# Kernel tuning notes

Measured on AMD Instinct MI355X. Metric: run time of the kernel, lower is better.

Reference implementation:

```python
import jax, jax.numpy as jnp
import numpy as np


def _gcn(A, x, W, b):
    # GCNConv(improved=True): add_remaining_self_loops(fill=2), symmetric normalization.
    n = A.shape[0]
    idx = jnp.arange(n)
    d = jnp.diagonal(A)
    Ahat = A.at[idx, idx].set(jnp.where(d == 0, 2.0, d))  # keep existing self-loop weights
    dinv = 1.0 / jnp.sqrt(Ahat.sum(axis=1))
    return (Ahat * dinv[:, None] * dinv[None, :]) @ (x @ W) + b


def _augment(A):
    # GraphUNet.augment_adj: add self loops, A @ A (spspmm), remove self loops.
    n = A.shape[0]
    idx = jnp.arange(n)
    A1 = A.at[idx, idx].add(1.0)
    return (A1 @ A1).at[idx, idx].set(0.0)


def _pool(A, x, p, k):
    # TopKPooling with tanh nonlinearity.
    score = jnp.tanh((x @ p) / jnp.linalg.norm(p))
    vals, perm = jax.lax.top_k(score, k)
    return A[perm][:, perm], x[perm] * vals[:, None], perm


def _gat(mask, x, W, a_src, a_dst, b, heads, c, concat):
    # GATConv, eval mode (attention dropout inactive). mask[dst, src] includes self loops.
    n = x.shape[0]
    h = (x @ W).reshape(n, heads, c)
    es = jnp.einsum('shc,hc->sh', h, a_src)
    ed = jnp.einsum('dhc,hc->dh', h, a_dst)
    logits = jax.nn.leaky_relu(ed[:, None, :] + es[None, :, :], 0.2)  # [dst, src, h]
    logits = jnp.where(mask[:, :, None], logits, jnp.finfo(logits.dtype).min)
    alpha = jax.nn.softmax(logits, axis=1)  # softmax over sources per destination
    out = jnp.einsum('dsh,shc->dhc', alpha, h)
    out = out.reshape(n, heads * c) if concat else out.mean(axis=1)
    return out + b


def setup_inputs() -> dict:
    key = jax.random.key(0)
    ks = jax.random.split(key, 34)
    N, E, IN, H, OUT, HEADS = 4096, 65536, 3, 64, 128, 4
    r = lambda k, s: jax.random.normal(k, s, jnp.float32) * 0.1
    inp = {}
    inp['x'] = jax.random.normal(ks[0], (N, IN), jnp.float32)
    inp['edge_index'] = jax.random.randint(ks[1], (2, E), 0, N)
    inp['unet_w0'] = r(ks[2], (IN, H)); inp['unet_b0'] = jnp.zeros((H,), jnp.float32)
    inp['unet_w1'] = r(ks[3], (H, H)); inp['unet_b1'] = jnp.zeros((H,), jnp.float32)
    inp['unet_w2'] = r(ks[4], (H, H)); inp['unet_b2'] = jnp.zeros((H,), jnp.float32)
    inp['unet_w3'] = r(ks[5], (H, H)); inp['unet_b3'] = jnp.zeros((H,), jnp.float32)
    inp['pool_p1'] = r(ks[6], (H,)); inp['pool_p2'] = r(ks[7], (H,)); inp['pool_p3'] = r(ks[8], (H,))
    inp['up_w0'] = r(ks[9], (H, H)); inp['up_b0'] = jnp.zeros((H,), jnp.float32)
    inp['up_w1'] = r(ks[10], (H, H)); inp['up_b1'] = jnp.zeros((H,), jnp.float32)
    inp['up_w2'] = r(ks[11], (H, OUT)); inp['up_b2'] = jnp.zeros((OUT,), jnp.float32)
    inp['ln_g'] = jnp.ones((OUT,), jnp.float32); inp['ln_b'] = jnp.zeros((OUT,), jnp.float32)
    inp['res_w'] = r(ks[12], (OUT, OUT)); inp['res_b'] = jnp.zeros((OUT,), jnp.float32)
    inp['gat1_w'] = r(ks[13], (OUT, HEADS * OUT))
    inp['gat1_asrc'] = r(ks[14], (HEADS, OUT)); inp['gat1_adst'] = r(ks[15], (HEADS, OUT))
    inp['gat1_b'] = jnp.zeros((HEADS * OUT,), jnp.float32)
    inp['gat2_w'] = r(ks[16], (HEADS * OUT, OUT))
    inp['gat2_asrc'] = r(ks[17], (1, OUT)); inp['gat2_adst'] = r(ks[18], (1, OUT))
    inp['gat2_b'] = jnp.zeros((OUT,), jnp.float32)
    return inp


def reference(x, edge_index, unet_w0, unet_b0, unet_w1, unet_b1, unet_w2, unet_b2,
              unet_w3, unet_b3, pool_p1, pool_p2, pool_p3, up_w0, up_b0, up_w1, up_b1,
              up_w2, up_b2, ln_g, ln_b, res_w, res_b, gat1_w, gat1_asrc, gat1_adst,
              gat1_b, gat2_w, gat2_asrc, gat2_adst, gat2_b):
    n0 = x.shape[0]
    # Dense weighted adjacency A[dst, src]; duplicate edges accumulate weight (scatter-add).
    A0 = jnp.zeros((n0, n0), x.dtype).at[edge_index[1], edge_index[0]].add(1.0)
    # ---- GraphUNet down path ----
    x0 = jax.nn.relu(_gcn(A0, x, unet_w0, unet_b0))
    k1 = (n0 + 1) // 2
    A1, h1, perm1 = _pool(_augment(A0), x0, pool_p1, k1)
    x1 = jax.nn.relu(_gcn(A1, h1, unet_w1, unet_b1))
    k2 = (k1 + 1) // 2
    A2, h2, perm2 = _pool(_augment(A1), x1, pool_p2, k2)
    x2 = jax.nn.relu(_gcn(A2, h2, unet_w2, unet_b2))
    k3 = (k2 + 1) // 2
    A3, h3, perm3 = _pool(_augment(A2), x2, pool_p3, k3)
    x3 = jax.nn.relu(_gcn(A3, h3, unet_w3, unet_b3))
    # ---- up path (sum_res=True) ----
    h = x2 + jnp.zeros_like(x2).at[perm3].set(x3)
    h = jax.nn.relu(_gcn(A2, h, up_w0, up_b0))
    h = x1 + jnp.zeros_like(x1).at[perm2].set(h)
    h = jax.nn.relu(_gcn(A1, h, up_w1, up_b1))
    h = x0 + jnp.zeros_like(x0).at[perm1].set(h)
    h = _gcn(A0, h, up_w2, up_b2)  # last up conv: no activation -> [n0, 128]
    # ---- LayerNorm(eps=1e-6) ----
    mu = h.mean(-1, keepdims=True)
    var = ((h - mu) ** 2).mean(-1, keepdims=True)
    u = (h - mu) / jnp.sqrt(var + 1e-6) * ln_g + ln_b
    residual = u @ res_w + res_b
    mask = (A0 > 0) | jnp.eye(n0, dtype=bool)  # GATConv adds self loops
    g = jax.nn.elu(_gat(mask, u, gat1_w, gat1_asrc, gat1_adst, gat1_b, 4, 128, True))
    g = _gat(mask, g, gat2_w, gat2_asrc, gat2_adst, gat2_b, 1, 128, False)
    return g + residual
```

## Files before the change

### kernel.cpp

```cpp
#include <hip/hip_runtime.h>
#include <math.h>


#define TPB 256
#define LDK 88
#define MAXN 128

typedef __attribute__((ext_vector_type(8))) short bf16x8;
typedef __attribute__((ext_vector_type(4))) float f32x4;

__device__ inline ushort f32_to_bf16(float v) {
    unsigned b = __float_as_uint(v);
    return (ushort)((b + 0x7FFF + ((b >> 16) & 1)) >> 16);
}
__device__ inline float bf2f(ushort u) { return __uint_as_float(((unsigned)u) << 16); }

__global__ void csr_init(int n, int* __restrict__ nbr, float* __restrict__ awt) {
    int id = blockIdx.x * TPB + threadIdx.x;
    if (id >= n * MAXN) return;
    int i = id >> 7, slot = id & (MAXN - 1);
    nbr[id] = (slot == 0) ? i : -1;
    awt[id] = (slot == 0) ? 1.0f : 0.0f;
}

__global__ void csr_insert(const int* __restrict__ ei, int E, int* __restrict__ nbr,
                           float* __restrict__ awt, int* __restrict__ deg,
                           int* __restrict__ diag) {
    int e = blockIdx.x * TPB + threadIdx.x;
    if (e >= E) return;
    int src = ei[e];
    int dst = ei[E + e];
    atomicAdd(&deg[dst], 1);
    if (src == dst) diag[src] = 1;
    int base = dst * MAXN;
    for (int p = 0; p < MAXN; ++p) {
        int cur = nbr[base + p];
        if (cur == src) { atomicAdd(&awt[base + p], 1.0f); break; }
        if (cur == -1) {
            int old = atomicCAS(&nbr[base + p], -1, src);
            if (old == -1 || old == src) { atomicAdd(&awt[base + p], 1.0f); break; }
        }
    }
}

__global__ void csr_finalize(const int* __restrict__ nbr, const int* __restrict__ deg,
                             const int* __restrict__ diag, int n, int* __restrict__ acnt,
                             float* __restrict__ dinv, float* __restrict__ selfw) {
    int i = blockIdx.x * TPB + threadIdx.x;
    if (i >= n) return;
    int cnt = 0;
    for (int p = 0; p < MAXN; ++p) {
        if (nbr[i * MAXN + p] == -1) break;
        ++cnt;
    }
    acnt[i] = cnt;
    float sw = diag[i] ? 0.f : 2.f;
    dinv[i] = 1.0f / sqrtf((float)deg[i] + sw);
    selfw[i] = sw;
}

__global__ void xw_gemm(const float* __restrict__ xin, const float* __restrict__ W,
                        float* __restrict__ C, int n, int fin, int f) {
    __shared__ float sW[64 * 128];
    int tid = threadIdx.x;
    for (int t = tid; t < fin * f; t += TPB) sW[t] = W[t];
    __syncthreads();
    int rpb = TPB / f;
    int r = blockIdx.x * rpb + tid / f;
    int c = tid - (tid / f) * f;
    if (r >= n) return;
    const float* xr = xin + (size_t)r * fin;
    float acc = 0.f;
    for (int k = 0; k < fin; ++k) acc += xr[k] * sW[k * f + c];
    C[(size_t)r * f + c] = acc;
}

__global__ void spmv_gcn(const int* __restrict__ nbr, const float* __restrict__ awt,
                         const int* __restrict__ acnt, const float* __restrict__ xw,
                         const float* __restrict__ dinv, const float* __restrict__ selfw,
                         const float* __restrict__ bias, float* __restrict__ out,
                         int f, int relu) {
    int i = blockIdx.x;
    int o = threadIdx.x;
    __shared__ int sj[MAXN];
    __shared__ float sw_[MAXN];
    int cnt = acnt[i];
    for (int a = o; a < cnt; a += blockDim.x) {
        sj[a] = nbr[i * MAXN + a];
        sw_[a] = awt[i * MAXN + a];
    }
    __syncthreads();
    if (o >= f) return;
    float sum = 0.f;
    for (int a = 0; a < cnt; ++a) {
        int j = sj[a];
        sum += sw_[a] * (xw[(size_t)j * f + o] * dinv[j]);
    }
    float yi = xw[(size_t)i * f + o] * dinv[i];
    sum -= yi;
    float v = dinv[i] * (sum + selfw[i] * yi) + bias[o];
    if (relu) v = fmaxf(v, 0.f);
    out[(size_t)i * f + o] = v;
}

__global__ void score_kernel2(const float* __restrict__ x, const float* __restrict__ p,
                              float* __restrict__ s, int n) {
    int i = blockIdx.x * TPB + threadIdx.x;
    if (i >= n) return;
    float a = 0.f, nrm = 0.f;
    for (int c = 0; c < 64; ++c) {
        float pc = p[c];
        nrm += pc * pc;
        a += x[(size_t)i * 64 + c] * pc;
    }
    s[i] = tanhf(a / sqrtf(nrm));
}

__global__ void rank_count(const float* __restrict__ s, int n, int* __restrict__ rank) {
    __shared__ float sj[256];
    int i = blockIdx.x * 256 + threadIdx.x;
    int j0 = blockIdx.y * 256;
    sj[threadIdx.x] = s[j0 + threadIdx.x];
    float si = s[i];
    __syncthreads();
    int r = 0;
#pragma unroll 8
    for (int jj = 0; jj < 256; ++jj) {
        float v = sj[jj];
        r += (v > si) || (v == si && (j0 + jj) < i);
    }
    atomicAdd(&rank[i], r);
}

__global__ void scatter_topk_all(const float* __restrict__ s, const int* __restrict__ rank,
                                 int n, int k, int* __restrict__ perm,
                                 float* __restrict__ vals, int* __restrict__ invp) {
    int i = blockIdx.x * TPB + threadIdx.x;
    if (i >= n) return;
    int r = rank[i];
    if (r < k) { perm[r] = i; vals[r] = s[i]; invp[i] = r; }
    else invp[i] = -1;
}

__global__ void gather_feat(const float* __restrict__ x, const int* __restrict__ perm,
                            const float* __restrict__ vals, int k, int f, float* __restrict__ h) {
    int id = blockIdx.x * TPB + threadIdx.x;
    if (id >= k * f) return;
    int r = id / f, c = id - r * f;
    h[id] = x[(size_t)perm[r] * f + c] * vals[r];
}

__global__ void spgemm_aug(const int* __restrict__ nbr, const float* __restrict__ awt,
                           const int* __restrict__ acnt, const int* __restrict__ perm,
                           const int* __restrict__ invp, int k,
                           ushort* __restrict__ Chi, ushort* __restrict__ Clo,
                           float* __restrict__ dinv, float* __restrict__ selfw) {
    __shared__ float row[2048];
    int r = blockIdx.x, tid = threadIdx.x;
    int pi = perm[r];
    for (int j = tid; j < k; j += TPB) row[j] = 0.f;
    __syncthreads();
    int cnt = acnt[pi];
    for (int a = 0; a < cnt; ++a) {
        int t = nbr[pi * MAXN + a];
        float w1 = awt[pi * MAXN + a];
        int c2 = acnt[t];
        for (int b = tid; b < c2; b += TPB) {
            int s = nbr[t * MAXN + b];
            int j = invp[s];
            if (j >= 0) atomicAdd(&row[j], w1 * awt[t * MAXN + b]);
        }
    }
    __syncthreads();
    float psum = 0.f;
    for (int j = tid; j < k; j += TPB) {
        float v = (j == r) ? 0.f : row[j];
        psum += v;
        ushort hi = f32_to_bf16(v);
        size_t o = (size_t)r * k + j;
        Chi[o] = hi;
        Clo[o] = f32_to_bf16(v - bf2f(hi));
    }
    for (int o = 32; o; o >>= 1) psum += __shfl_xor(psum, o);
    __shared__ float sh[4];
    if ((tid & 63) == 0) sh[tid >> 6] = psum;
    __syncthreads();
    if (tid == 0) {
        float tot = sh[0] + sh[1] + sh[2] + sh[3];
        dinv[r] = 1.0f / sqrtf(tot + 2.0f);
        selfw[r] = 2.0f;
    }
}

__global__ void transpose_aug_hl(const ushort* __restrict__ Ahi, const ushort* __restrict__ Alo,
                                 ushort* __restrict__ T, int n) {
    __shared__ float tile[64][65];
    int c0 = blockIdx.x * 64, r0 = blockIdx.y * 64;
    for (int t = threadIdx.x; t < 4096; t += TPB) {
        int r = t >> 6, c = t & 63;
        size_t o = (size_t)(r0 + r) * n + (c0 + c);
        float v = bf2f(Ahi[o]) + bf2f(Alo[o]);
        if (r0 + r == c0 + c) v += 1.0f;
        tile[c][r] = v;
    }
    __syncthreads();
    for (int t = threadIdx.x; t < 4096; t += TPB) {
        int c = t >> 6, r = t & 63;
        T[(size_t)(c0 + c) * n + (r0 + r)] = f32_to_bf16(tile[c][r]);
    }
}

__global__ void gather_rows_aug_hl(const ushort* __restrict__ Ahi, const ushort* __restrict__ Alo,
                                   const int* __restrict__ perm, ushort* __restrict__ Ag,
                                   int n, int rows) {
    int id = blockIdx.x * TPB + threadIdx.x;
    if (id >= rows * n) return;
    int r = id / n, t = id - r * n;
    int pr = perm[r];
    size_t o = (size_t)pr * n + t;
    float v = bf2f(Ahi[o]) + bf2f(Alo[o]);
    if (pr == t) v += 1.0f;
    Ag[id] = f32_to_bf16(v);
}

__global__ void gather_rows_u16(const ushort* __restrict__ T, const int* __restrict__ perm,
                                ushort* __restrict__ Bg, int n, int rows) {
    int id = blockIdx.x * TPB + threadIdx.x;
    if (id >= rows * n) return;
    int r = id / n, t = id - r * n;
    Bg[id] = T[(size_t)perm[r] * n + t];
}

__global__ void __launch_bounds__(256)
aug_gemm_acc(const ushort* __restrict__ Ag, const ushort* __restrict__ Bg,
             float* __restrict__ Caug, int K, int ldc, int kpb) {
    __shared__ __align__(16) ushort As[64 * LDK];
    __shared__ __align__(16) ushort Bs[64 * LDK];
    int tid = threadIdx.x;
    int wave = tid >> 6, lane = tid & 63;
    int wr = wave >> 1, wc = wave & 1;
    int m = lane & 15, quad = lane >> 4;
    int i0 = blockIdx.y * 64, j0 = blockIdx.x * 64;
    int kbeg = blockIdx.z * kpb;
    f32x4 acc[2][2];
#pragma unroll
    for (int a = 0; a < 2; ++a)
#pragma unroll
        for (int b = 0; b < 2; ++b) acc[a][b] = (f32x4){0.f, 0.f, 0.f, 0.f};
    const ushort* Ab = Ag + (size_t)i0 * K;
    const ushort* Bb = Bg + (size_t)j0 * K;
    for (int k0 = kbeg; k0 < kbeg + kpb; k0 += 64) {
#pragma unroll
        for (int v = 0; v < 2; ++v) {
            int idx = tid + (v << 8);
            int r = idx >> 3, c8 = idx & 7;
            *(uint4*)&As[r * LDK + c8 * 8] = *(const uint4*)&Ab[(size_t)r * K + k0 + c8 * 8];
            *(uint4*)&Bs[r * LDK + c8 * 8] = *(const uint4*)&Bb[(size_t)r * K + k0 + c8 * 8];
        }
        __syncthreads();
#pragma unroll
        for (int kk = 0; kk < 2; ++kk) {
            bf16x8 af[2], bfr[2];
#pragma unroll
            for (int mi = 0; mi < 2; ++mi)
                af[mi] = *(const bf16x8*)&As[(wr * 32 + mi * 16 + m) * LDK + kk * 32 + quad * 8];
#pragma unroll
            for (int ni = 0; ni < 2; ++ni)
                bfr[ni] = *(const bf16x8*)&Bs[(wc * 32 + ni * 16 + m) * LDK + kk * 32 + quad * 8];
#pragma unroll
            for (int mi = 0; mi < 2; ++mi)
#pragma unroll
                for (int ni = 0; ni < 2; ++ni)
                    acc[mi][ni] = __builtin_amdgcn_mfma_f32_16x16x32_bf16(
                        af[mi], bfr[ni], acc[mi][ni], 0, 0, 0);
        }
        __syncthreads();
    }
#pragma unroll
    for (int mi = 0; mi < 2; ++mi)
#pragma unroll
        for (int ni = 0; ni < 2; ++ni)
#pragma unroll
            for (int r = 0; r < 4; ++r) {
                int gi = i0 + wr * 32 + mi * 16 + quad * 4 + r;
                int gj = j0 + wc * 32 + ni * 16 + m;
                atomicAdd(&Caug[(size_t)gi * ldc + gj], acc[mi][ni][r]);
            }
}

__global__ void aug_finalize(const float* __restrict__ Caug, int k,
                             ushort* __restrict__ Chi, ushort* __restrict__ Clo,
                             float* __restrict__ dinv, float* __restrict__ selfw) {
    int r = blockIdx.x, tid = threadIdx.x;
    const float* row = Caug + (size_t)r * k;
    float psum = 0.f;
    for (int j = tid; j < k; j += TPB) {
        float v = (j == r) ? 0.f : row[j];
        psum += v;
        ushort hi = f32_to_bf16(v);
        size_t o = (size_t)r * k + j;
        Chi[o] = hi;
        Clo[o] = f32_to_bf16(v - bf2f(hi));
    }
    for (int o = 32; o; o >>= 1) psum += __shfl_xor(psum, o);
    __shared__ float sh[4];
    if ((tid & 63) == 0) sh[tid >> 6] = psum;
    __syncthreads();
    if (tid == 0) {
        float tot = sh[0] + sh[1] + sh[2] + sh[3];
        dinv[r] = 1.0f / sqrtf(tot + 2.0f);
        selfw[r] = 2.0f;
    }
}

__global__ void __launch_bounds__(256)
gcn_gemm(const ushort* __restrict__ Ahi, const ushort* __restrict__ Alo,
         const ushort* __restrict__ Bhi, const ushort* __restrict__ Blo,
         float* __restrict__ C, int K, int ldc, int kpb) {
    __shared__ __align__(16) ushort sAh[64 * LDK];
    __shared__ __align__(16) ushort sAl[64 * LDK];
    __shared__ __align__(16) ushort sBh[64 * LDK];
    __shared__ __align__(16) ushort sBl[64 * LDK];
    int tid = threadIdx.x;
    int wave = tid >> 6, lane = tid & 63;
    int wr = wave >> 1, wc = wave & 1;
    int m = lane & 15, quad = lane >> 4;
    int i0 = blockIdx.y * 64, j0 = blockIdx.x * 64;
    int kbeg = blockIdx.z * kpb;
    f32x4 acc[2][2];
#pragma unroll
    for (int a = 0; a < 2; ++a)
#pragma unroll
        for (int b = 0; b < 2; ++b) acc[a][b] = (f32x4){0.f, 0.f, 0.f, 0.f};
    for (int k0 = kbeg; k0 < kbeg + kpb; k0 += 64) {
#pragma unroll
        for (int v = 0; v < 2; ++v) {
            int idx = tid + (v << 8);
            int r = idx >> 3, c8 = idx & 7;
            size_t boff = (size_t)(j0 + r) * K + k0 + c8 * 8;
            *(uint4*)&sBh[r * LDK + c8 * 8] = *(const uint4*)&Bhi[boff];
            *(uint4*)&sBl[r * LDK + c8 * 8] = *(const uint4*)&Blo[boff];
            size_t aoff = (size_t)(i0 + r) * K + k0 + c8 * 8;
            *(uint4*)&sAh[r * LDK + c8 * 8] = *(const uint4*)&Ahi[aoff];
            *(uint4*)&sAl[r * LDK + c8 * 8] = *(const uint4*)&Alo[aoff];
        }
        __syncthreads();
#pragma unroll
        for (int kk = 0; kk < 2; ++kk) {
            bf16x8 ah[2], al[2], bh[2], bl[2];
#pragma unroll
            for (int mi = 0; mi < 2; ++mi) {
                ah[mi] = *(const bf16x8*)&sAh[(wr * 32 + mi * 16 + m) * LDK + kk * 32 + quad * 8];
                al[mi] = *(const bf16x8*)&sAl[(wr * 32 + mi * 16 + m) * LDK + kk * 32 + quad * 8];
            }
#pragma unroll
            for (int ni = 0; ni < 2; ++ni) {
                bh[ni] = *(const bf16x8*)&sBh[(wc * 32 + ni * 16 + m) * LDK + kk * 32 + quad * 8];
                bl[ni] = *(const bf16x8*)&sBl[(wc * 32 + ni * 16 + m) * LDK + kk * 32 + quad * 8];
            }
#pragma unroll
            for (int mi = 0; mi < 2; ++mi)
#pragma unroll
                for (int ni = 0; ni < 2; ++ni) {
                    acc[mi][ni] = __builtin_amdgcn_mfma_f32_16x16x32_bf16(ah[mi], bh[ni], acc[mi][ni], 0, 0, 0);
                    acc[mi][ni] = __builtin_amdgcn_mfma_f32_16x16x32_bf16(ah[mi], bl[ni], acc[mi][ni], 0, 0, 0);
                    acc[mi][ni] = __builtin_amdgcn_mfma_f32_16x16x32_bf16(al[mi], bh[ni], acc[mi][ni], 0, 0, 0);
                }
        }
        __syncthreads();
    }
#pragma unroll
    for (int mi = 0; mi < 2; ++mi)
#pragma unroll
        for (int ni = 0; ni < 2; ++ni)
#pragma unroll
            for (int r = 0; r < 4; ++r) {
                int gi = i0 + wr * 32 + mi * 16 + quad * 4 + r;
                int gj = j0 + wc * 32 + ni * 16 + m;
                atomicAdd(&C[(size_t)gi * ldc + gj], acc[mi][ni][r]);
            }
}

__global__ void build_yT_z(const float* __restrict__ xw, const float* __restrict__ dinv,
                           ushort* __restrict__ Bhi, ushort* __restrict__ Blo,
                           float* __restrict__ Cp, int n, int f) {
    __shared__ float t[64][65];
    int k0 = blockIdx.x * 64, c0 = blockIdx.y * 64;
#pragma unroll
    for (int v = 0; v < 16; ++v) {
        int idx = threadIdx.x + v * 256;
        int r = idx >> 6, c = idx & 63;
        t[r][c] = xw[(size_t)(k0 + r) * f + (c0 + c)] * dinv[k0 + r];
        Cp[(size_t)(k0 + r) * f + (c0 + c)] = 0.f;
    }
    __syncthreads();
#pragma unroll
    for (int v = 0; v < 16; ++v) {
        int idx = threadIdx.x + v * 256;
        int c = idx >> 6, k = idx & 63;
        float val = t[k][c];
        ushort hi = f32_to_bf16(val);
        size_t o = (size_t)(c0 + c) * n + (k0 + k);
        Bhi[o] = hi;
        Blo[o] = f32_to_bf16(val - bf2f(hi));
    }
}

__global__ void gcn_epilogue(const float* __restrict__ C, const float* __restrict__ xw,
                             const float* __restrict__ dinv, const float* __restrict__ selfw,
                             const float* __restrict__ b, float* __restrict__ out,
                             int n, int f, int relu) {
    int id = blockIdx.x * TPB + threadIdx.x;
    if (id >= n * f) return;
    int i = id / f, c = id - i * f;
    float y = xw[id] * dinv[i];
    float v = dinv[i] * (C[id] + selfw[i] * y) + b[c];
    if (relu) v = fmaxf(v, 0.f);
    out[id] = v;
}

__global__ void unpool_add(const float* __restrict__ xsrc, const float* __restrict__ h,
                           const int* __restrict__ invp, int n, int f, float* __restrict__ t) {
    int id = blockIdx.x * TPB + threadIdx.x;
    if (id >= n * f) return;
    int i = id / f, c = id - i * f;
    int r = invp[i];
    float v = xsrc[id];
    if (r >= 0) v += h[(size_t)r * f + c];
    t[id] = v;
}

__global__ void layernorm(const float* __restrict__ h, const float* __restrict__ g,
                          const float* __restrict__ b, float* __restrict__ u, int n) {
    int i = blockIdx.x;
    int t = threadIdx.x;
    float v = h[(size_t)i * 128 + t];
    __shared__ float s0[2], s1[2];
    float sum = v;
    for (int o = 32; o; o >>= 1) sum += __shfl_xor(sum, o);
    if ((t & 63) == 0) s0[t >> 6] = sum;
    __syncthreads();
    float mu = (s0[0] + s0[1]) * (1.0f / 128.0f);
    float d = v - mu;
    float sq = d * d;
    for (int o = 32; o; o >>= 1) sq += __shfl_xor(sq, o);
    if ((t & 63) == 0) s1[t >> 6] = sq;
    __syncthreads();
    float var = (s1[0] + s1[1]) * (1.0f / 128.0f);
    u[(size_t)i * 128 + t] = d / sqrtf(var + 1e-6f) * g[t] + b[t];
}

__global__ void transpose_split(const float* __restrict__ W, ushort* __restrict__ Bhi,
                                ushort* __restrict__ Blo, int K, int N) {
    __shared__ float tile[64][65];
    int n0 = blockIdx.x * 64, k0 = blockIdx.y * 64;
    for (int t = threadIdx.x; t < 4096; t += TPB) {
        int r = t >> 6, c = t & 63;
        tile[r][c] = W[(size_t)(k0 + r) * N + (n0 + c)];
    }
    __syncthreads();
    for (int t = threadIdx.x; t < 4096; t += TPB) {
        int c = t >> 6, r = t & 63;
        float v = tile[r][c];
        ushort hi = f32_to_bf16(v);
        size_t o = (size_t)(n0 + c) * K + (k0 + r);
        Bhi[o] = hi;
        Blo[o] = f32_to_bf16(v - bf2f(hi));
    }
}

__global__ void __launch_bounds__(256)
gemm_bt_store(const float* __restrict__ A, const ushort* __restrict__ Bhi,
              const ushort* __restrict__ Blo, const float* __restrict__ bias,
              float* __restrict__ C, int K, int N) {
    __shared__ __align__(16) ushort sAh[64 * LDK];
    __shared__ __align__(16) ushort sAl[64 * LDK];
    __shared__ __align__(16) ushort sBh[64 * LDK];
    __shared__ __align__(16) ushort sBl[64 * LDK];
    int tid = threadIdx.x;
    int wave = tid >> 6, lane = tid & 63;
    int wr = wave >> 1, wc = wave & 1;
    int m = lane & 15, quad = lane >> 4;
    int i0 = blockIdx.y * 64, j0 = blockIdx.x * 64;
    f32x4 acc[2][2];
#pragma unroll
    for (int a = 0; a < 2; ++a)
#pragma unroll
        for (int b = 0; b < 2; ++b) acc[a][b] = (f32x4){0.f, 0.f, 0.f, 0.f};
    for (int k0 = 0; k0 < K; k0 += 64) {
#pragma unroll
        for (int v = 0; v < 2; ++v) {
            int idx = tid + (v << 8);
            int r = idx >> 3, c8 = idx & 7;
            size_t boff = (size_t)(j0 + r) * K + k0 + c8 * 8;
            *(uint4*)&sBh[r * LDK + c8 * 8] = *(const uint4*)&Bhi[boff];
            *(uint4*)&sBl[r * LDK + c8 * 8] = *(const uint4*)&Blo[boff];
            size_t aoff = (size_t)(i0 + r) * K + k0 + c8 * 8;
            float4 fa = *(const float4*)&A[aoff];
            float4 fb = *(const float4*)&A[aoff + 4];
            ushort h0 = f32_to_bf16(fa.x), h1 = f32_to_bf16(fa.y);
            ushort h2 = f32_to_bf16(fa.z), h3 = f32_to_bf16(fa.w);
            ushort h4 = f32_to_bf16(fb.x), h5 = f32_to_bf16(fb.y);
            ushort h6 = f32_to_bf16(fb.z), h7 = f32_to_bf16(fb.w);
            uint4 ph, pl;
            ph.x = (uint)h0 | ((uint)h1 << 16);
            ph.y = (uint)h2 | ((uint)h3 << 16);
            ph.z = (uint)h4 | ((uint)h5 << 16);
            ph.w = (uint)h6 | ((uint)h7 << 16);
            pl.x = (uint)f32_to_bf16(fa.x - bf2f(h0)) | ((uint)f32_to_bf16(fa.y - bf2f(h1)) << 16);
            pl.y = (uint)f32_to_bf16(fa.z - bf2f(h2)) | ((uint)f32_to_bf16(fa.w - bf2f(h3)) << 16);
            pl.z = (uint)f32_to_bf16(fb.x - bf2f(h4)) | ((uint)f32_to_bf16(fb.y - bf2f(h5)) << 16);
            pl.w = (uint)f32_to_bf16(fb.z - bf2f(h6)) | ((uint)f32_to_bf16(fb.w - bf2f(h7)) << 16);
            *(uint4*)&sAh[r * LDK + c8 * 8] = ph;
            *(uint4*)&sAl[r * LDK + c8 * 8] = pl;
        }
        __syncthreads();
#pragma unroll
        for (int kk = 0; kk < 2; ++kk) {
            bf16x8 ah[2], al[2], bh[2], bl[2];
#pragma unroll
            for (int mi = 0; mi < 2; ++mi) {
                ah[mi] = *(const bf16x8*)&sAh[(wr * 32 + mi * 16 + m) * LDK + kk * 32 + quad * 8];
                al[mi] = *(const bf16x8*)&sAl[(wr * 32 + mi * 16 + m) * LDK + kk * 32 + quad * 8];
            }
#pragma unroll
            for (int ni = 0; ni < 2; ++ni) {
                bh[ni] = *(const bf16x8*)&sBh[(wc * 32 + ni * 16 + m) * LDK + kk * 32 + quad * 8];
                bl[ni] = *(const bf16x8*)&sBl[(wc * 32 + ni * 16 + m) * LDK + kk * 32 + quad * 8];
            }
#pragma unroll
            for (int mi = 0; mi < 2; ++mi)
#pragma unroll
                for (int ni = 0; ni < 2; ++ni) {
                    acc[mi][ni] = __builtin_amdgcn_mfma_f32_16x16x32_bf16(ah[mi], bh[ni], acc[mi][ni], 0, 0, 0);
                    acc[mi][ni] = __builtin_amdgcn_mfma_f32_16x16x32_bf16(ah[mi], bl[ni], acc[mi][ni], 0, 0, 0);
                    acc[mi][ni] = __builtin_amdgcn_mfma_f32_16x16x32_bf16(al[mi], bh[ni], acc[mi][ni], 0, 0, 0);
                }
        }
        __syncthreads();
    }
#pragma unroll
    for (int mi = 0; mi < 2; ++mi)
#pragma unroll
        for (int ni = 0; ni < 2; ++ni)
#pragma unroll
            for (int r = 0; r < 4; ++r) {
                int gi = i0 + wr * 32 + mi * 16 + quad * 4 + r;
                int gj = j0 + wc * 32 + ni * 16 + m;
                float v = acc[mi][ni][r];
                if (bias) v += bias[gj];
                C[(size_t)gi * N + gj] = v;
            }
}

__global__ void __launch_bounds__(256)
gemm_bt_split(const float* __restrict__ A, const ushort* __restrict__ Bhi,
              const ushort* __restrict__ Blo, float* __restrict__ C,
              int K, int N, int kpb) {
    __shared__ __align__(16) ushort sAh[64 * LDK];
    __shared__ __align__(16) ushort sAl[64 * LDK];
    __shared__ __align__(16) ushort sBh[64 * LDK];
    __shared__ __align__(16) ushort sBl[64 * LDK];
    int tid = threadIdx.x;
    int wave = tid >> 6, lane = tid & 63;
    int wr = wave >> 1, wc = wave & 1;
    int m = lane & 15, quad = lane >> 4;
    int i0 = blockIdx.y * 64, j0 = blockIdx.x * 64;
    int kbeg = blockIdx.z * kpb;
    f32x4 acc[2][2];
#pragma unroll
    for (int a = 0; a < 2; ++a)
#pragma unroll
        for (int b = 0; b < 2; ++b) acc[a][b] = (f32x4){0.f, 0.f, 0.f, 0.f};
    for (int k0 = kbeg; k0 < kbeg + kpb; k0 += 64) {
#pragma unroll
        for (int v = 0; v < 2; ++v) {
            int idx = tid + (v << 8);
            int r = idx >> 3, c8 = idx & 7;
            size_t boff = (size_t)(j0 + r) * K + k0 + c8 * 8;
            *(uint4*)&sBh[r * LDK + c8 * 8] = *(const uint4*)&Bhi[boff];
            *(uint4*)&sBl[r * LDK + c8 * 8] = *(const uint4*)&Blo[boff];
            size_t aoff = (size_t)(i0 + r) * K + k0 + c8 * 8;
            float4 fa = *(const float4*)&A[aoff];
            float4 fb = *(const float4*)&A[aoff + 4];
            ushort h0 = f32_to_bf16(fa.x), h1 = f32_to_bf16(fa.y);
            ushort h2 = f32_to_bf16(fa.z), h3 = f32_to_bf16(fa.w);
            ushort h4 = f32_to_bf16(fb.x), h5 = f32_to_bf16(fb.y);
            ushort h6 = f32_to_bf16(fb.z), h7 = f32_to_bf16(fb.w);
            uint4 ph, pl;
            ph.x = (uint)h0 | ((uint)h1 << 16);
            ph.y = (uint)h2 | ((uint)h3 << 16);
            ph.z = (uint)h4 | ((uint)h5 << 16);
            ph.w = (uint)h6 | ((uint)h7 << 16);
            pl.x = (uint)f32_to_bf16(fa.x - bf2f(h0)) | ((uint)f32_to_bf16(fa.y - bf2f(h1)) << 16);
            pl.y = (uint)f32_to_bf16(fa.z - bf2f(h2)) | ((uint)f32_to_bf16(fa.w - bf2f(h3)) << 16);
            pl.z = (uint)f32_to_bf16(fb.x - bf2f(h4)) | ((uint)f32_to_bf16(fb.y - bf2f(h5)) << 16);
            pl.w = (uint)f32_to_bf16(fb.z - bf2f(h6)) | ((uint)f32_to_bf16(fb.w - bf2f(h7)) << 16);
            *(uint4*)&sAh[r * LDK + c8 * 8] = ph;
            *(uint4*)&sAl[r * LDK + c8 * 8] = pl;
        }
        __syncthreads();
#pragma unroll
        for (int kk = 0; kk < 2; ++kk) {
            bf16x8 ah[2], al[2], bh[2], bl[2];
#pragma unroll
            for (int mi = 0; mi < 2; ++mi) {
                ah[mi] = *(const bf16x8*)&sAh[(wr * 32 + mi * 16 + m) * LDK + kk * 32 + quad * 8];
                al[mi] = *(const bf16x8*)&sAl[(wr * 32 + mi * 16 + m) * LDK + kk * 32 + quad * 8];
            }
#pragma unroll
            for (int ni = 0; ni < 2; ++ni) {
                bh[ni] = *(const bf16x8*)&sBh[(wc * 32 + ni * 16 + m) * LDK + kk * 32 + quad * 8];
                bl[ni] = *(const bf16x8*)&sBl[(wc * 32 + ni * 16 + m) * LDK + kk * 32 + quad * 8];
            }
#pragma unroll
            for (int mi = 0; mi < 2; ++mi)
#pragma unroll
                for (int ni = 0; ni < 2; ++ni) {
                    acc[mi][ni] = __builtin_amdgcn_mfma_f32_16x16x32_bf16(ah[mi], bh[ni], acc[mi][ni], 0, 0, 0);
                    acc[mi][ni] = __builtin_amdgcn_mfma_f32_16x16x32_bf16(ah[mi], bl[ni], acc[mi][ni], 0, 0, 0);
                    acc[mi][ni] = __builtin_amdgcn_mfma_f32_16x16x32_bf16(al[mi], bh[ni], acc[mi][ni], 0, 0, 0);
                }
        }
        __syncthreads();
    }
#pragma unroll
    for (int mi = 0; mi < 2; ++mi)
#pragma unroll
        for (int ni = 0; ni < 2; ++ni)
#pragma unroll
            for (int r = 0; r < 4; ++r) {
                int gi = i0 + wr * 32 + mi * 16 + quad * 4 + r;
                int gj = j0 + wc * 32 + ni * 16 + m;
                atomicAdd(&C[(size_t)gi * N + gj], acc[mi][ni][r]);
            }
}

__global__ void attn_coef2(const float* __restrict__ hf, const float* __restrict__ asrc,
                           const float* __restrict__ adst, float* __restrict__ es,
                           float* __restrict__ ed, int heads) {
    int j = blockIdx.x;
    int wave = threadIdx.x >> 6, lane = threadIdx.x & 63;
    if (wave >= heads) return;
    const float* hp = hf + (size_t)j * heads * 128 + wave * 128;
    float v0 = hp[lane], v1 = hp[lane + 64];
    float a = v0 * asrc[wave * 128 + lane] + v1 * asrc[wave * 128 + lane + 64];
    float d = v0 * adst[wave * 128 + lane] + v1 * adst[wave * 128 + lane + 64];
    for (int o = 32; o; o >>= 1) { a += __shfl_xor(a, o); d += __shfl_xor(d, o); }
    if (lane == 0) { es[j * heads + wave] = a; ed[j * heads + wave] = d; }
}

__global__ void gat_sparse(const int* __restrict__ nbr, const int* __restrict__ ncnt, int n,
                           const float* __restrict__ hf, const float* __restrict__ es,
                           const float* __restrict__ ed, const float* __restrict__ bias,
                           const float* __restrict__ resid, float* __restrict__ out,
                           int heads, int mode) {
    int i = blockIdx.x;
    int tid = threadIdx.x;
    __shared__ int idx[MAXN];
    __shared__ float lg[MAXN * 4];
    __shared__ float hmax[4], hsum[4];
    int m = ncnt[i];
    for (int t = tid; t < m; t += TPB) idx[t] = nbr[i * MAXN + t];
    __syncthreads();
    for (int t = tid; t < m * heads; t += TPB) {
        int jl = t / heads, h = t - jl * heads;
        float l = ed[i * heads + h] + es[idx[jl] * heads + h];
        lg[jl * heads + h] = (l > 0.f) ? l : 0.2f * l;
    }
    __syncthreads();
    int h = tid >> 6, lane = tid & 63;
    if (h < heads) {
        float mx = -3.4e38f;
        for (int jl = lane; jl < m; jl += 64) mx = fmaxf(mx, lg[jl * heads + h]);
        for (int o = 32; o; o >>= 1) mx = fmaxf(mx, __shfl_xor(mx, o));
        if (lane == 0) hmax[h] = mx;
    }
    __syncthreads();
    if (h < heads) {
        float mx = hmax[h];
        float sm = 0.f;
        for (int jl = lane; jl < m; jl += 64) {
            float p = expf(lg[jl * heads + h] - mx);
            lg[jl * heads + h] = p;
            sm += p;
        }
        for (int o = 32; o; o >>= 1) sm += __shfl_xor(sm, o);
        if (lane == 0) hsum[h] = sm;
    }
    __syncthreads();
    int width = heads * 128;
    for (int o = tid; o < width; o += TPB) {
        int hh = o >> 7;
        float acc = 0.f;
        for (int jl = 0; jl < m; ++jl)
            acc += lg[jl * heads + hh] * hf[(size_t)idx[jl] * width + o];
        float v = acc / hsum[hh] + bias[o];
        if (mode == 0) v = (v > 0.f) ? v : expm1f(v);
        else v += resid[(size_t)i * width + o];
        out[(size_t)i * width + o] = v;
    }
}

static inline int cdiv(int a, int b) { return (a + b - 1) / b; }

static int pick_z(int gx, int gy, int K) {
    int z = 1;
    while (gx * gy * z < 384 && K / (2 * z) >= 64) z <<= 1;
    return z;
}

static void run_gcn_dense(hipStream_t stream, const ushort* Ahi, const ushort* Alo,
                          int n, const float* xin, int fin,
                          const float* W, const float* bias, int f,
                          const float* dinv, const float* selfw,
                          float* xw, ushort* yThi, ushort* yTlo, float* Cp,
                          float* out, int relu) {
    xw_gemm<<<cdiv(n, TPB / f), TPB, 0, stream>>>(xin, W, xw, n, fin, f);
    build_yT_z<<<dim3(n / 64, f / 64), TPB, 0, stream>>>(xw, dinv, yThi, yTlo, Cp, n, f);
    int z = pick_z(f / 64, n / 64, n);
    gcn_gemm<<<dim3(f / 64, n / 64, z), TPB, 0, stream>>>(Ahi, Alo, yThi, yTlo, Cp, n, f, n / z);
    gcn_epilogue<<<cdiv(n * f, TPB), TPB, 0, stream>>>(Cp, xw, dinv, selfw, bias, out, n, f, relu);
}

static void run_gcn_sparse(hipStream_t stream, const int* nbr, const float* awt,
                           const int* acnt, int n, const float* xin, int fin,
                           const float* W, const float* bias, int f,
                           const float* dinv, const float* selfw,
                           float* xw, float* out, int relu) {
    xw_gemm<<<cdiv(n, TPB / f), TPB, 0, stream>>>(xin, W, xw, n, fin, f);
    spmv_gcn<<<n, f, 0, stream>>>(nbr, awt, acnt, xw, dinv, selfw, bias, out, f, relu);
}

static void run_topk(hipStream_t stream, const float* score, int n, int k, int* rank,
                     int* perm, float* vals, int* invp) {
    hipMemsetAsync(rank, 0, n * sizeof(int), stream);
    rank_count<<<dim3(n / 256, n / 256), 256, 0, stream>>>(score, n, rank);
    scatter_topk_all<<<cdiv(n, TPB), TPB, 0, stream>>>(score, rank, n, k, perm, vals, invp);
}

static void run_aug_dense(hipStream_t stream, const ushort* Ahi, const ushort* Alo, int n,
                          const int* perm, int k, ushort* Tbf, ushort* Agb, ushort* Bgb,
                          float* Caug, ushort* Chi, ushort* Clo, float* dinv, float* selfw) {
    transpose_aug_hl<<<dim3(n / 64, n / 64), TPB, 0, stream>>>(Ahi, Alo, Tbf, n);
    gather_rows_aug_hl<<<cdiv(k * n, TPB), TPB, 0, stream>>>(Ahi, Alo, perm, Agb, n, k);
    gather_rows_u16<<<cdiv(k * n, TPB), TPB, 0, stream>>>(Tbf, perm, Bgb, n, k);
    hipMemsetAsync(Caug, 0, (size_t)k * k * sizeof(float), stream);
    int z = 8;
    aug_gemm_acc<<<dim3(k / 64, k / 64, z), TPB, 0, stream>>>(Agb, Bgb, Caug, n, k, n / z);
    aug_finalize<<<k, TPB, 0, stream>>>(Caug, k, Chi, Clo, dinv, selfw);
}

extern "C" void kernel_launch(void* const* d_in, const int* in_sizes, int n_in,
                              void* d_out, int out_size, void* d_ws, size_t ws_size,
                              hipStream_t stream) {
    const float* x   = (const float*)d_in[0];
    const int*   ei  = (const int*)d_in[1];
    const float* w0  = (const float*)d_in[2];  const float* b0  = (const float*)d_in[3];
    const float* w1  = (const float*)d_in[4];  const float* b1  = (const float*)d_in[5];
    const float* w2  = (const float*)d_in[6];  const float* b2  = (const float*)d_in[7];
    const float* w3  = (const float*)d_in[8];  const float* b3  = (const float*)d_in[9];
    const float* p1  = (const float*)d_in[10];
    const float* p2  = (const float*)d_in[11];
    const float* p3  = (const float*)d_in[12];
    const float* uw0 = (const float*)d_in[13]; const float* ub0 = (const float*)d_in[14];
    const float* uw1 = (const float*)d_in[15]; const float* ub1 = (const float*)d_in[16];
    const float* uw2 = (const float*)d_in[17]; const float* ub2 = (const float*)d_in[18];
    const float* lng = (const float*)d_in[19]; const float* lnb = (const float*)d_in[20];
    const float* rw  = (const float*)d_in[21]; const float* rb  = (const float*)d_in[22];
    const float* g1w = (const float*)d_in[23];
    const float* g1as = (const float*)d_in[24]; const float* g1ad = (const float*)d_in[25];
    const float* g1b = (const float*)d_in[26];
    const float* g2w = (const float*)d_in[27];
    const float* g2as = (const float*)d_in[28]; const float* g2ad = (const float*)d_in[29];
    const float* g2b = (const float*)d_in[30];

    const int N = 4096, E = 65536;
    const int K1 = 2048, K2 = 1024, K3 = 512;

    float* base = (float*)d_ws;
    size_t off = 0;
    auto alloc = [&](size_t nf) { float* p = base + off; off += (nf + 63) & ~(size_t)63; return p; };

    ushort* A1hi = (ushort*)alloc((size_t)K1 * K1 / 2);
    ushort* A1lo = (ushort*)alloc((size_t)K1 * K1 / 2);
    ushort* A2hi = (ushort*)alloc((size_t)K2 * K2 / 2);
    ushort* A2lo = (ushort*)alloc((size_t)K2 * K2 / 2);
    ushort* A3hi = (ushort*)alloc((size_t)K3 * K3 / 2);
    ushort* A3lo = (ushort*)alloc((size_t)K3 * K3 / 2);
    ushort* Tbf  = (ushort*)alloc((size_t)K1 * K1 / 2);
    ushort* Agb  = (ushort*)alloc((size_t)K2 * K1 / 2);
    ushort* Bgb  = (ushort*)alloc((size_t)K2 * K1 / 2);
    ushort* yThi = (ushort*)alloc((size_t)128 * N / 2);
    ushort* yTlo = (ushort*)alloc((size_t)128 * N / 2);
    ushort* Whi  = (ushort*)alloc((size_t)512 * 128 / 2);
    ushort* Wlo  = (ushort*)alloc((size_t)512 * 128 / 2);
    float* Caug  = alloc((size_t)K2 * K2);
    float* Cp    = alloc((size_t)N * 128);
    float* x0    = alloc((size_t)N * 64);
    float* x1    = alloc((size_t)K1 * 64);
    float* x2    = alloc((size_t)K2 * 64);
    float* x3    = alloc((size_t)K3 * 64);
    float* h1    = alloc((size_t)K1 * 64);
    float* h2    = alloc((size_t)K2 * 64);
    float* h3    = alloc((size_t)K3 * 64);
    float* xw    = alloc((size_t)N * 128);
    float* dinv0 = alloc(N);  float* selfw0 = alloc(N);
    float* dinv1 = alloc(K1); float* selfw1 = alloc(K1);
    float* dinv2 = alloc(K2); float* selfw2 = alloc(K2);
    float* dinv3 = alloc(K3); float* selfw3 = alloc(K3);
    int*   deg   = (int*)alloc(2 * N);
    int*   diag  = deg + N;
    float* score = alloc(N);
    int*   rank  = (int*)alloc(N);
    float* vals1 = alloc(K1); float* vals2 = alloc(K2); float* vals3 = alloc(K3);
    int*   perm1 = (int*)alloc(K1); int* perm2 = (int*)alloc(K2); int* perm3 = (int*)alloc(K3);
    int*   invp1 = (int*)alloc(N);  int* invp2 = (int*)alloc(K1); int* invp3 = (int*)alloc(K2);
    int*   nbr   = (int*)alloc((size_t)N * MAXN);
    float* awt   = alloc((size_t)N * MAXN);
    int*   acnt  = (int*)alloc(N);
    float* t2    = alloc((size_t)K2 * 64);
    float* t1    = alloc((size_t)K1 * 64);
    float* t0    = alloc((size_t)N * 64);
    float* hfin  = alloc((size_t)N * 128);
    float* u     = alloc((size_t)N * 128);
    float* resid = alloc((size_t)N * 128);
    float* hf1   = alloc((size_t)N * 512);
    float* es1   = alloc((size_t)N * 4); float* ed1 = alloc((size_t)N * 4);
    float* g1    = alloc((size_t)N * 512);
    float* hf2   = alloc((size_t)N * 128);
    float* es2   = alloc(N); float* ed2 = alloc(N);
    (void)ws_size; (void)n_in; (void)in_sizes; (void)out_size;

    csr_init<<<cdiv(N * MAXN, TPB), TPB, 0, stream>>>(N, nbr, awt);
    hipMemsetAsync(deg, 0, 2 * N * sizeof(int), stream);
    csr_insert<<<cdiv(E, TPB), TPB, 0, stream>>>(ei, E, nbr, awt, deg, diag);
    csr_finalize<<<cdiv(N, TPB), TPB, 0, stream>>>(nbr, deg, diag, N, acnt, dinv0, selfw0);

    run_gcn_sparse(stream, nbr, awt, acnt, N, x, 3, w0, b0, 64, dinv0, selfw0, xw, x0, 1);

    score_kernel2<<<cdiv(N, TPB), TPB, 0, stream>>>(x0, p1, score, N);
    run_topk(stream, score, N, K1, rank, perm1, vals1, invp1);
    spgemm_aug<<<K1, TPB, 0, stream>>>(nbr, awt, acnt, perm1, invp1, K1,
                                       A1hi, A1lo, dinv1, selfw1);
    gather_feat<<<cdiv(K1 * 64, TPB), TPB, 0, stream>>>(x0, perm1, vals1, K1, 64, h1);
    run_gcn_dense(stream, A1hi, A1lo, K1, h1, 64, w1, b1, 64,
                  dinv1, selfw1, xw, yThi, yTlo, Cp, x1, 1);

    score_kernel2<<<cdiv(K1, TPB), TPB, 0, stream>>>(x1, p2, score, K1);
    run_topk(stream, score, K1, K2, rank, perm2, vals2, invp2);
    run_aug_dense(stream, A1hi, A1lo, K1, perm2, K2, Tbf, Agb, Bgb, Caug,
                  A2hi, A2lo, dinv2, selfw2);
    gather_feat<<<cdiv(K2 * 64, TPB), TPB, 0, stream>>>(x1, perm2, vals2, K2, 64, h2);
    run_gcn_dense(stream, A2hi, A2lo, K2, h2, 64, w2, b2, 64,
                  dinv2, selfw2, xw, yThi, yTlo, Cp, x2, 1);

    score_kernel2<<<cdiv(K2, TPB), TPB, 0, stream>>>(x2, p3, score, K2);
    run_topk(stream, score, K2, K3, rank, perm3, vals3, invp3);
    run_aug_dense(stream, A2hi, A2lo, K2, perm3, K3, Tbf, Agb, Bgb, Caug,
                  A3hi, A3lo, dinv3, selfw3);
    gather_feat<<<cdiv(K3 * 64, TPB), TPB, 0, stream>>>(x2, perm3, vals3, K3, 64, h3);
    run_gcn_dense(stream, A3hi, A3lo, K3, h3, 64, w3, b3, 64,
                  dinv3, selfw3, xw, yThi, yTlo, Cp, x3, 1);

    unpool_add<<<cdiv(K2 * 64, TPB), TPB, 0, stream>>>(x2, x3, invp3, K2, 64, t2);
    run_gcn_dense(stream, A2hi, A2lo, K2, t2, 64, uw0, ub0, 64,
                  dinv2, selfw2, xw, yThi, yTlo, Cp, h2, 1);

    unpool_add<<<cdiv(K1 * 64, TPB), TPB, 0, stream>>>(x1, h2, invp2, K1, 64, t1);
    run_gcn_dense(stream, A1hi, A1lo, K1, t1, 64, uw1, ub1, 64,
                  dinv1, selfw1, xw, yThi, yTlo, Cp, h1, 1);

    unpool_add<<<cdiv(N * 64, TPB), TPB, 0, stream>>>(x0, h1, invp1, N, 64, t0);
    run_gcn_sparse(stream, nbr, awt, acnt, N, t0, 64, uw2, ub2, 128,
                   dinv0, selfw0, xw, hfin, 0);

    layernorm<<<N, 128, 0, stream>>>(hfin, lng, lnb, u, N);
    transpose_split<<<dim3(2, 2), TPB, 0, stream>>>(rw, Whi, Wlo, 128, 128);
    gemm_bt_store<<<dim3(2, N / 64), TPB, 0, stream>>>(u, Whi, Wlo, rb, resid, 128, 128);

    transpose_split<<<dim3(8, 2), TPB, 0, stream>>>(g1w, Whi, Wlo, 128, 512);
    gemm_bt_store<<<dim3(8, N / 64), TPB, 0, stream>>>(u, Whi, Wlo, nullptr, hf1, 128, 512);
    attn_coef2<<<N, 256, 0, stream>>>(hf1, g1as, g1ad, es1, ed1, 4);
    gat_sparse<<<N, TPB, 0, stream>>>(nbr, acnt, N, hf1, es1, ed1, g1b, nullptr, g1, 4, 0);

    transpose_split<<<dim3(2, 8), TPB, 0, stream>>>(g2w, Whi, Wlo, 512, 128);
    hipMemsetAsync(hf2, 0, (size_t)N * 128 * sizeof(float), stream);
    gemm_bt_split<<<dim3(2, N / 64, 4), TPB, 0, stream>>>(g1, Whi, Wlo, hf2, 512, 128, 128);
    attn_coef2<<<N, 64, 0, stream>>>(hf2, g2as, g2ad, es2, ed2, 1);
    gat_sparse<<<N, TPB, 0, stream>>>(nbr, acnt, N, hf2, es2, ed2, g2b, resid, (float*)d_out, 1, 1);
}
```

Measured before the change: 546.8 us.

## Build adjacency CSR via atomic bucket scatter plus per-row dedup

Replaces the linear-probe CAS insertion into fixed-width adjacency rows with a two-step build. First each edge is appended to a per-destination bucket using one atomic cursor increment. Then one 64-thread block per node deduplicates its bucket in shared memory, computing weights, the self-loop flag and the degree normalisation. This removes serialized probe loops, CAS contention and the full-table init pass, at the cost of an O(d^2) dedup per row and an extra bucket buffer.

```diff
diff --git a/kernel.cpp b/kernel.cpp
--- a/kernel.cpp
+++ b/kernel.cpp
@@ -15,48 +15,58 @@
 }
 __device__ inline float bf2f(ushort u) { return __uint_as_float(((unsigned)u) << 16); }
 
-__global__ void csr_init(int n, int* __restrict__ nbr, float* __restrict__ awt) {
-    int id = blockIdx.x * TPB + threadIdx.x;
-    if (id >= n * MAXN) return;
-    int i = id >> 7, slot = id & (MAXN - 1);
-    nbr[id] = (slot == 0) ? i : -1;
-    awt[id] = (slot == 0) ? 1.0f : 0.0f;
-}
-
-__global__ void csr_insert(const int* __restrict__ ei, int E, int* __restrict__ nbr,
-                           float* __restrict__ awt, int* __restrict__ deg,
-                           int* __restrict__ diag) {
+__global__ void bucket_scatter(const int* __restrict__ ei, int E, int* __restrict__ buck,
+                               int* __restrict__ cursor) {
     int e = blockIdx.x * TPB + threadIdx.x;
     if (e >= E) return;
     int src = ei[e];
     int dst = ei[E + e];
-    atomicAdd(&deg[dst], 1);
-    if (src == dst) diag[src] = 1;
-    int base = dst * MAXN;
-    for (int p = 0; p < MAXN; ++p) {
-        int cur = nbr[base + p];
-        if (cur == src) { atomicAdd(&awt[base + p], 1.0f); break; }
-        if (cur == -1) {
-            int old = atomicCAS(&nbr[base + p], -1, src);
-            if (old == -1 || old == src) { atomicAdd(&awt[base + p], 1.0f); break; }
-        }
-    }
-}
-
-__global__ void csr_finalize(const int* __restrict__ nbr, const int* __restrict__ deg,
-                             const int* __restrict__ diag, int n, int* __restrict__ acnt,
-                             float* __restrict__ dinv, float* __restrict__ selfw) {
-    int i = blockIdx.x * TPB + threadIdx.x;
-    if (i >= n) return;
-    int cnt = 0;
-    for (int p = 0; p < MAXN; ++p) {
-        if (nbr[i * MAXN + p] == -1) break;
-        ++cnt;
-    }
-    acnt[i] = cnt;
-    float sw = diag[i] ? 0.f : 2.f;
-    dinv[i] = 1.0f / sqrtf((float)deg[i] + sw);
-    selfw[i] = sw;
+    int pos = atomicAdd(&cursor[dst], 1);
+    if (pos < MAXN) buck[dst * MAXN + pos] = src;
+}
+
+__global__ void build_csr(const int* __restrict__ buck, const int* __restrict__ cursor,
+                          int n, int* __restrict__ nbr, float* __restrict__ awt,
+                          int* __restrict__ acnt, float* __restrict__ dinv,
+                          float* __restrict__ selfw) {
+    int i = blockIdx.x;
+    int tid = threadIdx.x;
+    __shared__ int s[MAXN];
+    __shared__ int outcnt, selfFound;
+    int raw = cursor[i];
+    int d = min(raw, MAXN);
+    if (tid == 0) { outcnt = 0; selfFound = 0; }
+    for (int p = tid; p < d; p += 64) s[p] = buck[i * MAXN + p];
+    __syncthreads();
+    for (int p = tid; p < d; p += 64)
+        if (s[p] == i) atomicOr(&selfFound, 1);
+    __syncthreads();
+    for (int p = tid; p < d; p += 64) {
+        int v = s[p];
+        bool first = true;
+        for (int q = 0; q < p; ++q)
+            if (s[q] == v) { first = false; break; }
+        if (first) {
+            int w = 1;
+            for (int q = p + 1; q < d; ++q) w += (s[q] == v);
+            int slot = atomicAdd(&outcnt, 1);
+            nbr[i * MAXN + slot] = v;
+            awt[i * MAXN + slot] = (float)w + (v == i ? 1.0f : 0.0f);
+        }
+    }
+    __syncthreads();
+    if (tid == 0) {
+        int cnt = outcnt;
+        if (!selfFound && cnt < MAXN) {
+            nbr[i * MAXN + cnt] = i;
+            awt[i * MAXN + cnt] = 1.0f;
+            ++cnt;
+        }
+        acnt[i] = cnt;
+        float sw = selfFound ? 0.f : 2.f;
+        dinv[i] = 1.0f / sqrtf((float)raw + sw);
+        selfw[i] = sw;
+    }
 }
 
 __global__ void xw_gemm(const float* __restrict__ xin, const float* __restrict__ W,
@@ -809,8 +819,8 @@
     float* dinv1 = alloc(K1); float* selfw1 = alloc(K1);
     float* dinv2 = alloc(K2); float* selfw2 = alloc(K2);
     float* dinv3 = alloc(K3); float* selfw3 = alloc(K3);
-    int*   deg   = (int*)alloc(2 * N);
-    int*   diag  = deg + N;
+    int*   cursor= (int*)alloc(N);
+    int*   buck  = (int*)alloc((size_t)N * MAXN);
     float* score = alloc(N);
     int*   rank  = (int*)alloc(N);
     float* vals1 = alloc(K1); float* vals2 = alloc(K2); float* vals3 = alloc(K3);
@@ -832,10 +842,9 @@
     float* es2   = alloc(N); float* ed2 = alloc(N);
     (void)ws_size; (void)n_in; (void)in_sizes; (void)out_size;
 
-    csr_init<<<cdiv(N * MAXN, TPB), TPB, 0, stream>>>(N, nbr, awt);
-    hipMemsetAsync(deg, 0, 2 * N * sizeof(int), stream);
-    csr_insert<<<cdiv(E, TPB), TPB, 0, stream>>>(ei, E, nbr, awt, deg, diag);
-    csr_finalize<<<cdiv(N, TPB), TPB, 0, stream>>>(nbr, deg, diag, N, acnt, dinv0, selfw0);
+    hipMemsetAsync(cursor, 0, N * sizeof(int), stream);
+    bucket_scatter<<<cdiv(E, TPB), TPB, 0, stream>>>(ei, E, buck, cursor);
+    build_csr<<<N, 64, 0, stream>>>(buck, cursor, N, nbr, awt, acnt, dinv0, selfw0);
 
     run_gcn_sparse(stream, nbr, awt, acnt, N, x, 3, w0, b0, 64, dinv0, selfw0, xw, x0, 1);
 
```

Result: faster. 486.5 us (-11.0%).
